# Kernel optimization log

Hardware: AMD Instinct MI355X
Metric: run time of the kernel (lower is better)

## Reference

```python
import jax, jax.numpy as jnp
import numpy as np

F_DIM = 256; L = 4; B = 1; H = 160; W = 160; FH = 1024; N = B * H * W

def _ln(x, w, b):
    mu = jnp.mean(x, -1, keepdims=True)
    var = jnp.mean(jnp.square(x - mu), -1, keepdims=True)
    return (x - mu) * jax.lax.rsqrt(var + 1e-5) * w + b

def _conv(x, w, b, groups=1, pad=0):
    y = jax.lax.conv_general_dilated(x, w, (1, 1), [(pad, pad), (pad, pad)],
                                     dimension_numbers=('NCHW', 'OIHW', 'NCHW'),
                                     feature_group_count=groups)
    return y + b[None, :, None, None]

def _wsilu(x):
    return jax.nn.sigmoid(4.0 * x) * x

def setup_inputs() -> dict:
    key = jax.random.key(0)
    ks = iter(jax.random.split(key, 40))
    nk = lambda: next(ks)
    s = 1.0 / np.sqrt(F_DIM).astype(np.float32)
    inp = {}
    inp['x'] = jax.random.normal(nk(), (B, 1, H, W), jnp.float32)
    inp['cin_w1'] = jax.random.normal(nk(), (F_DIM, 1, 1, 1), jnp.float32)
    inp['cin_b1'] = jnp.zeros((F_DIM,), jnp.float32)
    inp['cin_w2'] = jax.random.normal(nk(), (F_DIM, 1, 7, 7), jnp.float32) * 0.15
    inp['cin_b2'] = jnp.zeros((F_DIM,), jnp.float32)
    inp['ln0_w'] = jnp.ones((F_DIM,), jnp.float32); inp['ln0_b'] = jnp.zeros((F_DIM,), jnp.float32)
    inp['ln1_w'] = jnp.ones((L, F_DIM), jnp.float32); inp['ln1_b'] = jnp.zeros((L, F_DIM), jnp.float32)
    inp['ln2_w'] = jnp.ones((L, F_DIM), jnp.float32); inp['ln2_b'] = jnp.zeros((L, F_DIM), jnp.float32)
    for n in ['att_tmk', 'att_tmv', 'att_tmr', 'ffn_tmk', 'ffn_tmr']:
        inp[n] = jax.random.uniform(nk(), (L, F_DIM), jnp.float32)
    inp['att_tf'] = jax.random.normal(nk(), (L, F_DIM), jnp.float32) * 0.5
    # time_decay is stored as -exp(raw) by the module's loader
    inp['att_td'] = -jnp.exp(jax.random.normal(nk(), (L, F_DIM), jnp.float32) * 0.5)
    for n in ['att_kw', 'att_vw', 'att_rw', 'att_ow', 'ffn_rw']:
        inp[n] = jax.random.normal(nk(), (L, F_DIM, F_DIM), jnp.float32) * s
    inp['ffn_kw'] = jax.random.normal(nk(), (L, FH, F_DIM), jnp.float32) * s
    inp['ffn_vw'] = jax.random.normal(nk(), (L, F_DIM, FH), jnp.float32) * (1.0 / np.sqrt(FH).astype(np.float32))
    inp['spa_dw_w'] = jax.random.normal(nk(), (L, F_DIM, 1, 7, 7), jnp.float32) * 0.15
    inp['spa_dw_b'] = jnp.zeros((L, F_DIM), jnp.float32)
    inp['spa_pw_w'] = jax.random.normal(nk(), (L, F_DIM, F_DIM, 1, 1), jnp.float32) * s
    inp['spa_pw_b'] = jnp.zeros((L, F_DIM), jnp.float32)
    st = jnp.zeros((5 * L, N, F_DIM), jnp.float32)
    st = st.at[4::5].add(-1e30)  # pp slots start at -1e30 as in torch init
    inp['state0'] = st
    return inp

def reference(x, cin_w1, cin_b1, cin_w2, cin_b2, ln0_w, ln0_b, ln1_w, ln1_b,
              ln2_w, ln2_b, att_tmk, att_tmv, att_tmr, att_tf, att_td,
              att_kw, att_vw, att_rw, att_ow, ffn_tmk, ffn_tmr, ffn_kw,
              ffn_vw, ffn_rw, spa_dw_w, spa_dw_b, spa_pw_w, spa_pw_b, state0):
    # conv stem: 1x1 -> depthwise 7x7 -> WSiLU
    d = _conv(x, cin_w1, cin_b1)
    d = _wsilu(_conv(d, cin_w2, cin_b2, groups=F_DIM, pad=3))
    d = d.transpose(0, 2, 3, 1).reshape(N, F_DIM)  # 'b f h w -> (b h w) f'
    for i in range(L):
        if i == 0:
            d = _ln(d, ln0_w, ln0_b)
        # --- SA: single-step RWKV WKV ---
        xs = _ln(d, ln1_w[i], ln1_b[i])
        sp = state0[5 * i + 1]
        aa = state0[5 * i + 2]; bb = state0[5 * i + 3]; pp = state0[5 * i + 4]
        xk = xs * att_tmk[i] + sp * (1 - att_tmk[i])
        xv = xs * att_tmv[i] + sp * (1 - att_tmv[i])
        xr = xs * att_tmr[i] + sp * (1 - att_tmr[i])
        r = jax.nn.sigmoid(xr @ att_rw[i].T)
        k = xk @ att_kw[i].T
        v = xv @ att_vw[i].T
        ww = att_tf[i] + k
        p = jnp.maximum(pp, ww)
        e1 = jnp.exp(pp - p); e2 = jnp.exp(ww - p)
        wkv = (e1 * aa + e2 * v) / (e1 * bb + e2)
        d = d + (r * wkv) @ att_ow[i].T
        # --- FF: squared-relu channel mix ---
        xs = _ln(d, ln2_w[i], ln2_b[i])
        sp = state0[5 * i + 0]
        xk = xs * ffn_tmk[i] + sp * (1 - ffn_tmk[i])
        xr = xs * ffn_tmr[i] + sp * (1 - ffn_tmr[i])
        rr = jax.nn.sigmoid(xr @ ffn_rw[i].T)
        kk = jnp.square(jax.nn.relu(xk @ ffn_kw[i].T))
        d = d + rr * (kk @ ffn_vw[i].T)
        # --- spatial residual block ---
        img = d.reshape(B, H, W, F_DIM).transpose(0, 3, 1, 2)
        img = img + _conv(_conv(img, spa_dw_w[i], spa_dw_b[i], groups=F_DIM, pad=3),
                          spa_pw_w[i], spa_pw_b[i])
        d = img.transpose(0, 2, 3, 1).reshape(N, F_DIM)
    return d.reshape(B, H, W, F_DIM).transpose(0, 3, 1, 2)
```

## Files before the change

### kernel.cpp

```cpp
#include <hip/hip_runtime.h>
#include <hip/hip_bf16.h>
#include <cstdint>
#include <cstddef>

#define F_DIMC 256
#define FHC    1024
#define IMGH   160
#define IMGW   160
#define NTOK   25600
#define NLAY   4

using bf16 = __hip_bfloat16;
using f16  = _Float16;
typedef __attribute__((ext_vector_type(8))) short bf16x8;
typedef __attribute__((ext_vector_type(4))) float f32x4;

#define MFMA16(a, b, c) __builtin_amdgcn_mfma_f32_16x16x32_bf16((a), (b), (c), 0, 0, 0)

union H4 { f16 h[4]; uint2 u; };
union Pack4 { bf16 h[4]; uint2 u; };

struct Cvt6 { const float* s[6]; bf16* d[6]; };
__global__ void cvt6_k(Cvt6 a, int n) {
    int z = blockIdx.y;
    int i = blockIdx.x * 256 + threadIdx.x;
    if (i < n) a.d[z][i] = __float2bfloat16(a.s[z][i]);
}
struct Cvt2 { const float* s[2]; bf16* d[2]; };
__global__ void cvt2_k(Cvt2 a, int n) {
    int z = blockIdx.y;
    int i = blockIdx.x * 256 + threadIdx.x;
    if (i < n) a.d[z][i] = __float2bfloat16(a.s[z][i]);
}

__global__ void dw_transpose_k(const float* __restrict__ src, float* __restrict__ dst, int n) {
    int i = blockIdx.x * 256 + threadIdx.x;
    if (i < n) {
        int f = i & (F_DIMC - 1);
        int lt = i >> 8;
        int t = lt % 49;
        int l = lt / 49;
        dst[i] = src[((size_t)l * F_DIMC + f) * 49 + t];
    }
}

__global__ __launch_bounds__(256)
void stem2_k(const float* __restrict__ x, const float* __restrict__ w1,
             const float* __restrict__ b1, const float* __restrict__ w2,
             const float* __restrict__ b2, f16* __restrict__ d)
{
    __shared__ float wts[49][64];
    __shared__ float w1s[64], b1s[64], b2s[64];
    __shared__ float2 xp[7][22];
    const int tid = threadIdx.x;
    const int f0 = blockIdx.y * 64;
    const int y = blockIdx.x / 10;
    const int x0 = (blockIdx.x % 10) * 16;

    for (int idx = tid; idx < 49 * 64; idx += 256) {
        int t = idx >> 6, fl = idx & 63;
        wts[t][fl] = w2[(f0 + fl) * 49 + t];
    }
    if (tid < 64) {
        w1s[tid] = w1[f0 + tid];
        b1s[tid] = b1[f0 + tid];
        b2s[tid] = b2[f0 + tid];
    }
    for (int p = tid; p < 7 * 22; p += 256) {
        int py = p / 22, px = p % 22;
        int gy = y + py - 3, gx = x0 + px - 3;
        bool ok = (unsigned)gy < IMGH && (unsigned)gx < IMGW;
        xp[py][px] = ok ? make_float2(x[gy * IMGW + gx], 1.f) : make_float2(0.f, 0.f);
    }
    __syncthreads();

    const int fl = tid & 63;
    const int xbase = (tid >> 6) * 4;
    float acc[4] = {0.f, 0.f, 0.f, 0.f}, accw[4] = {0.f, 0.f, 0.f, 0.f};
    #pragma unroll
    for (int ky = 0; ky < 7; ++ky) {
        float2 row[10];
        #pragma unroll
        for (int q = 0; q < 10; ++q) row[q] = xp[ky][xbase + q];
        #pragma unroll
        for (int kx = 0; kx < 7; ++kx) {
            float w = wts[ky * 7 + kx][fl];
            #pragma unroll
            for (int j = 0; j < 4; ++j) {
                acc[j]  = fmaf(row[j + kx].x, w, acc[j]);
                accw[j] = fmaf(row[j + kx].y, w, accw[j]);
            }
        }
    }
    const float w1f = w1s[fl], b1f = b1s[fl], b2f = b2s[fl];
    #pragma unroll
    for (int j = 0; j < 4; ++j) {
        float u = fmaf(w1f, acc[j], fmaf(b1f, accw[j], b2f));
        int pix = y * IMGW + x0 + xbase + j;
        d[(size_t)pix * F_DIMC + f0 + fl] = (f16)(u / (1.f + __expf(-4.f * u)));
    }
}

__device__ __forceinline__ void wave_ln(float* x, const float* __restrict__ w,
                                        const float* __restrict__ b, int lane)
{
    float s = x[0] + x[1] + x[2] + x[3];
    #pragma unroll
    for (int m = 1; m < 64; m <<= 1) s += __shfl_xor(s, m, 64);
    float mu = s * 0.00390625f;
    float t0 = x[0] - mu, t1 = x[1] - mu, t2 = x[2] - mu, t3 = x[3] - mu;
    float v = t0 * t0 + t1 * t1 + t2 * t2 + t3 * t3;
    #pragma unroll
    for (int m = 1; m < 64; m <<= 1) v += __shfl_xor(v, m, 64);
    float inv = rsqrtf(v * 0.00390625f + 1e-5f);
    f32x4 wv = *(const f32x4*)(w + lane * 4);
    f32x4 bv = *(const f32x4*)(b + lane * 4);
    x[0] = t0 * inv * wv[0] + bv[0];
    x[1] = t1 * inv * wv[1] + bv[1];
    x[2] = t2 * inv * wv[2] + bv[2];
    x[3] = t3 * inv * wv[3] + bv[3];
}

template<bool LN0>
__global__ __launch_bounds__(256)
void lnmix_sa_k(f16* __restrict__ d, const float* __restrict__ sp,
                const float* __restrict__ ln0w, const float* __restrict__ ln0b,
                const float* __restrict__ lnw, const float* __restrict__ lnb,
                const float* __restrict__ tmk, const float* __restrict__ tmv,
                const float* __restrict__ tmr,
                bf16* __restrict__ xk, bf16* __restrict__ xv, bf16* __restrict__ xr)
{
    const int lane = threadIdx.x & 63;
    const int n = blockIdx.x * 4 + (threadIdx.x >> 6);
    const int base = n * F_DIMC + lane * 4;
    H4 hv; hv.u = *(const uint2*)(d + base);
    float xo[4] = {(float)hv.h[0], (float)hv.h[1], (float)hv.h[2], (float)hv.h[3]};
    if (LN0) {
        wave_ln(xo, ln0w, ln0b, lane);
        H4 o;
        #pragma unroll
        for (int j = 0; j < 4; ++j) o.h[j] = (f16)xo[j];
        *(uint2*)(d + base) = o.u;
    }
    float xs[4] = {xo[0], xo[1], xo[2], xo[3]};
    wave_ln(xs, lnw, lnb, lane);
    f32x4 spv = *(const f32x4*)(sp + base);
    f32x4 k4 = *(const f32x4*)(tmk + lane * 4);
    f32x4 v4 = *(const f32x4*)(tmv + lane * 4);
    f32x4 r4 = *(const f32x4*)(tmr + lane * 4);
    Pack4 pk, pv, pr;
    #pragma unroll
    for (int j = 0; j < 4; ++j) {
        pk.h[j] = __float2bfloat16(xs[j] * k4[j] + spv[j] * (1.f - k4[j]));
        pv.h[j] = __float2bfloat16(xs[j] * v4[j] + spv[j] * (1.f - v4[j]));
        pr.h[j] = __float2bfloat16(xs[j] * r4[j] + spv[j] * (1.f - r4[j]));
    }
    *(uint2*)(xk + base) = pk.u;
    *(uint2*)(xv + base) = pv.u;
    *(uint2*)(xr + base) = pr.u;
}

__global__ __launch_bounds__(256)
void lnmix_ff_k(const f16* __restrict__ d, const float* __restrict__ sp,
                const float* __restrict__ lnw, const float* __restrict__ lnb,
                const float* __restrict__ tmk, const float* __restrict__ tmr,
                bf16* __restrict__ xk, bf16* __restrict__ xr)
{
    const int lane = threadIdx.x & 63;
    const int n = blockIdx.x * 4 + (threadIdx.x >> 6);
    const int base = n * F_DIMC + lane * 4;
    H4 hv; hv.u = *(const uint2*)(d + base);
    float xs[4] = {(float)hv.h[0], (float)hv.h[1], (float)hv.h[2], (float)hv.h[3]};
    wave_ln(xs, lnw, lnb, lane);
    f32x4 spv = *(const f32x4*)(sp + base);
    f32x4 k4 = *(const f32x4*)(tmk + lane * 4);
    f32x4 r4 = *(const f32x4*)(tmr + lane * 4);
    Pack4 pk, pr;
    #pragma unroll
    for (int j = 0; j < 4; ++j) {
        pk.h[j] = __float2bfloat16(xs[j] * k4[j] + spv[j] * (1.f - k4[j]));
        pr.h[j] = __float2bfloat16(xs[j] * r4[j] + spv[j] * (1.f - r4[j]));
    }
    *(uint2*)(xk + base) = pk.u;
    *(uint2*)(xr + base) = pr.u;
}

__global__ __launch_bounds__(256)
void wkv_k(const f16* __restrict__ r_, const f16* __restrict__ k_,
           const f16* __restrict__ v_, const float* __restrict__ aa,
           const float* __restrict__ bb, const float* __restrict__ pp,
           const float* __restrict__ tf, bf16* __restrict__ out)
{
    int i = blockIdx.x * 256 + threadIdx.x;
    int f0 = (i << 2) & (F_DIMC - 1);
    H4 r4; r4.u = *(const uint2*)(r_ + (size_t)i * 4);
    H4 k4; k4.u = *(const uint2*)(k_ + (size_t)i * 4);
    H4 v4; v4.u = *(const uint2*)(v_ + (size_t)i * 4);
    f32x4 a4 = *(const f32x4*)(aa + (size_t)i * 4);
    f32x4 b4 = *(const f32x4*)(bb + (size_t)i * 4);
    f32x4 p4 = *(const f32x4*)(pp + (size_t)i * 4);
    f32x4 t4 = *(const f32x4*)(tf + f0);
    Pack4 po;
    #pragma unroll
    for (int j = 0; j < 4; ++j) {
        float ww = t4[j] + (float)k4.h[j];
        float p = fmaxf(p4[j], ww);
        float e1 = __expf(p4[j] - p);
        float e2 = __expf(ww - p);
        float wkv = (e1 * a4[j] + e2 * (float)v4.h[j]) / (e1 * b4[j] + e2);
        po.h[j] = __float2bfloat16((float)r4.h[j] * wkv);
    }
    *(uint2*)(out + (size_t)i * 4) = po.u;
}

__device__ __forceinline__ void stage_swz16(const bf16* __restrict__ g, int lda,
                                            bf16* lds, int tid)
{
    #pragma unroll
    for (int s = 0; s < 8; ++s) {
        int chunk = s * 256 + tid;
        int row = chunk >> 4, c16 = chunk & 15;
        int gc = c16 ^ (row & 15);
        __builtin_amdgcn_global_load_lds(
            (const __attribute__((address_space(1))) void*)(g + (size_t)row * lda + gc * 8),
            (__attribute__((address_space(3))) void*)(lds + chunk * 8), 16, 0, 0);
    }
}

template<int RB>
__device__ __forceinline__ bf16x8 frag_ld(const bf16* lds, int row, int cb)
{
    return *(const bf16x8*)((const char*)lds + row * RB + (cb ^ ((row & 15) << 4)));
}

struct G3 { const bf16* A[3]; const bf16* W[3]; f16* C[3]; };
__global__ __launch_bounds__(256, 2)
void gemm3_k(G3 g)
{
    __shared__ __align__(16) bf16 As[128 * 128];
    __shared__ __align__(16) bf16 Bs[128 * 128];
    const int z = blockIdx.z;
    const bf16* __restrict__ A  = g.A[z];
    const bf16* __restrict__ Bw = g.W[z];
    f16* __restrict__ C         = g.C[z];
    const int tid = threadIdx.x, lane = tid & 63, wave = tid >> 6;
    const int wr = wave >> 1, wc = wave & 1;
    const int lr = lane & 15, hi = lane >> 4;
    const int m0 = blockIdx.x * 128, n0 = blockIdx.y * 128;

    f32x4 acc[4][4];
    #pragma unroll
    for (int m = 0; m < 4; ++m)
        #pragma unroll
        for (int n = 0; n < 4; ++n) acc[m][n] = (f32x4){0.f, 0.f, 0.f, 0.f};

    #pragma unroll
    for (int kt = 0; kt < 256; kt += 128) {
        stage_swz16(A + (size_t)m0 * 256 + kt, 256, As, tid);
        stage_swz16(Bw + (size_t)n0 * 256 + kt, 256, Bs, tid);
        __syncthreads();
        #pragma unroll
        for (int ks = 0; ks < 4; ++ks) {
            int cb = ks * 64 + hi * 16;
            bf16x8 a[4], b[4];
            #pragma unroll
            for (int mf = 0; mf < 4; ++mf) a[mf] = frag_ld<256>(As, wr * 64 + mf * 16 + lr, cb);
            #pragma unroll
            for (int nf = 0; nf < 4; ++nf) b[nf] = frag_ld<256>(Bs, wc * 64 + nf * 16 + lr, cb);
            #pragma unroll
            for (int mf = 0; mf < 4; ++mf)
                #pragma unroll
                for (int nf = 0; nf < 4; ++nf)
                    acc[mf][nf] = MFMA16(a[mf], b[nf], acc[mf][nf]);
        }
        __syncthreads();
    }

    const int lr0 = hi * 4;
    #pragma unroll
    for (int mf = 0; mf < 4; ++mf)
        #pragma unroll
        for (int nf = 0; nf < 4; ++nf) {
            int col = n0 + wc * 64 + nf * 16 + lr;
            #pragma unroll
            for (int j = 0; j < 4; ++j) {
                int row = m0 + wr * 64 + mf * 16 + lr0 + j;
                float v = acc[mf][nf][j];
                if (z == 2) v = 1.f / (1.f + __expf(-v));
                C[(size_t)row * F_DIMC + col] = (f16)v;
            }
        }
}

template<int EPI, int K>
__global__ __launch_bounds__(256, 2)
void gemm128_k(const bf16* __restrict__ A, const bf16* __restrict__ Bw,
               int Nout, f16* __restrict__ Cf, bf16* __restrict__ Cb,
               const float* __restrict__ bias)
{
    __shared__ __align__(16) bf16 As[128 * 128];
    __shared__ __align__(16) bf16 Bs[128 * 128];
    const int tid = threadIdx.x, lane = tid & 63, wave = tid >> 6;
    const int wr = wave >> 1, wc = wave & 1;
    const int lr = lane & 15, hi = lane >> 4;
    const int m0 = blockIdx.x * 128, n0 = blockIdx.y * 128;

    f32x4 acc[4][4];
    #pragma unroll
    for (int m = 0; m < 4; ++m)
        #pragma unroll
        for (int n = 0; n < 4; ++n) acc[m][n] = (f32x4){0.f, 0.f, 0.f, 0.f};

    #pragma unroll
    for (int kt = 0; kt < K; kt += 128) {
        stage_swz16(A + (size_t)m0 * K + kt, K, As, tid);
        stage_swz16(Bw + (size_t)n0 * K + kt, K, Bs, tid);
        __syncthreads();
        #pragma unroll
        for (int ks = 0; ks < 4; ++ks) {
            int cb = ks * 64 + hi * 16;
            bf16x8 a[4], b[4];
            #pragma unroll
            for (int mf = 0; mf < 4; ++mf) a[mf] = frag_ld<256>(As, wr * 64 + mf * 16 + lr, cb);
            #pragma unroll
            for (int nf = 0; nf < 4; ++nf) b[nf] = frag_ld<256>(Bs, wc * 64 + nf * 16 + lr, cb);
            #pragma unroll
            for (int mf = 0; mf < 4; ++mf)
                #pragma unroll
                for (int nf = 0; nf < 4; ++nf)
                    acc[mf][nf] = MFMA16(a[mf], b[nf], acc[mf][nf]);
        }
        __syncthreads();
    }

    const int lr0 = hi * 4;
    #pragma unroll
    for (int mf = 0; mf < 4; ++mf)
        #pragma unroll
        for (int nf = 0; nf < 4; ++nf) {
            int col = n0 + wc * 64 + nf * 16 + lr;
            #pragma unroll
            for (int j = 0; j < 4; ++j) {
                int row = m0 + wr * 64 + mf * 16 + lr0 + j;
                size_t cidx = (size_t)row * Nout + col;
                float v = acc[mf][nf][j];
                if constexpr (EPI == 2) { float t = fmaxf(v, 0.f); Cb[cidx] = __float2bfloat16(t * t); }
                else if constexpr (EPI == 3) Cf[cidx] = (f16)((float)Cf[cidx] + v);
                else if constexpr (EPI == 5) Cf[cidx] = (f16)((float)Cf[cidx] + v + bias[col]);
            }
        }
}

__global__ __launch_bounds__(256, 2)
void fvwrr_k(const bf16* __restrict__ kkb, const bf16* __restrict__ fvw,
             const bf16* __restrict__ xr, const bf16* __restrict__ rw,
             f16* __restrict__ d)
{
    __shared__ __align__(16) bf16 As[128 * 128];
    __shared__ __align__(16) bf16 Bs[128 * 128];
    const int tid = threadIdx.x, lane = tid & 63, wave = tid >> 6;
    const int wr = wave >> 1, wc = wave & 1;
    const int lr = lane & 15, hi = lane >> 4;
    const int m0 = blockIdx.x * 128, n0 = blockIdx.y * 128;

    f32x4 arr[4][4], am[4][4];
    #pragma unroll
    for (int m = 0; m < 4; ++m)
        #pragma unroll
        for (int n = 0; n < 4; ++n) {
            arr[m][n] = (f32x4){0.f, 0.f, 0.f, 0.f};
            am[m][n]  = (f32x4){0.f, 0.f, 0.f, 0.f};
        }

    #pragma unroll
    for (int kt = 0; kt < 256; kt += 128) {
        stage_swz16(xr + (size_t)m0 * 256 + kt, 256, As, tid);
        stage_swz16(rw + (size_t)n0 * 256 + kt, 256, Bs, tid);
        __syncthreads();
        #pragma unroll
        for (int ks = 0; ks < 4; ++ks) {
            int cb = ks * 64 + hi * 16;
            bf16x8 a[4], b[4];
            #pragma unroll
            for (int mf = 0; mf < 4; ++mf) a[mf] = frag_ld<256>(As, wr * 64 + mf * 16 + lr, cb);
            #pragma unroll
            for (int nf = 0; nf < 4; ++nf) b[nf] = frag_ld<256>(Bs, wc * 64 + nf * 16 + lr, cb);
            #pragma unroll
            for (int mf = 0; mf < 4; ++mf)
                #pragma unroll
                for (int nf = 0; nf < 4; ++nf)
                    arr[mf][nf] = MFMA16(a[mf], b[nf], arr[mf][nf]);
        }
        __syncthreads();
    }
    #pragma unroll
    for (int kt = 0; kt < 1024; kt += 128) {
        stage_swz16(kkb + (size_t)m0 * 1024 + kt, 1024, As, tid);
        stage_swz16(fvw + (size_t)n0 * 1024 + kt, 1024, Bs, tid);
        __syncthreads();
        #pragma unroll
        for (int ks = 0; ks < 4; ++ks) {
            int cb = ks * 64 + hi * 16;
            bf16x8 a[4], b[4];
            #pragma unroll
            for (int mf = 0; mf < 4; ++mf) a[mf] = frag_ld<256>(As, wr * 64 + mf * 16 + lr, cb);
            #pragma unroll
            for (int nf = 0; nf < 4; ++nf) b[nf] = frag_ld<256>(Bs, wc * 64 + nf * 16 + lr, cb);
            #pragma unroll
            for (int mf = 0; mf < 4; ++mf)
                #pragma unroll
                for (int nf = 0; nf < 4; ++nf)
                    am[mf][nf] = MFMA16(a[mf], b[nf], am[mf][nf]);
        }
        __syncthreads();
    }

    const int lr0 = hi * 4;
    #pragma unroll
    for (int mf = 0; mf < 4; ++mf)
        #pragma unroll
        for (int nf = 0; nf < 4; ++nf) {
            int col = n0 + wc * 64 + nf * 16 + lr;
            #pragma unroll
            for (int j = 0; j < 4; ++j) {
                int row = m0 + wr * 64 + mf * 16 + lr0 + j;
                size_t cidx = (size_t)row * F_DIMC + col;
                float rr = 1.f / (1.f + __expf(-arr[mf][nf][j]));
                d[cidx] = (f16)((float)d[cidx] + rr * am[mf][nf][j]);
            }
        }
}

__global__ __launch_bounds__(256)
void dwconv2_k(const f16* __restrict__ d, const float* __restrict__ wT,
               const float* __restrict__ bias, bf16* __restrict__ out)
{
    __shared__ float patch[196][64];
    __shared__ float wt[49][64];
    const int lane = threadIdx.x;
    const int ty = threadIdx.y;
    const int f0 = blockIdx.z * 64;
    const int w0 = blockIdx.x * 8, h0 = blockIdx.y * 8;

    for (int t = ty; t < 49; t += 4) wt[t][lane] = wT[t * F_DIMC + f0 + lane];
    for (int p = ty; p < 196; p += 4) {
        int py = p / 14, px = p % 14;
        int gy = h0 + py - 3, gx = w0 + px - 3;
        float v = 0.f;
        if ((unsigned)gy < IMGH && (unsigned)gx < IMGW)
            v = (float)d[(size_t)(gy * IMGW + gx) * F_DIMC + f0 + lane];
        patch[p][lane] = v;
    }
    __syncthreads();

    const float b = bias[f0 + lane];
    #pragma unroll
    for (int rr = 0; rr < 2; ++rr) {
        int ry = ty * 2 + rr;
        float acc8[8];
        #pragma unroll
        for (int px = 0; px < 8; ++px) acc8[px] = b;
        #pragma unroll
        for (int ky = 0; ky < 7; ++ky) {
            float rowv[14];
            #pragma unroll
            for (int c = 0; c < 14; ++c) rowv[c] = patch[(ry + ky) * 14 + c][lane];
            #pragma unroll
            for (int kx = 0; kx < 7; ++kx) {
                float w = wt[ky * 7 + kx][lane];
                #pragma unroll
                for (int px = 0; px < 8; ++px)
                    acc8[px] = fmaf(rowv[px + kx], w, acc8[px]);
            }
        }
        #pragma unroll
        for (int px = 0; px < 8; ++px)
            out[(size_t)((h0 + ry) * IMGW + (w0 + px)) * F_DIMC + f0 + lane] = __float2bfloat16(acc8[px]);
    }
}

__global__ __launch_bounds__(256)
void transpose_out_k(const f16* __restrict__ d, float* __restrict__ out)
{
    __shared__ float tile[32][33];
    const int n0 = blockIdx.x * 32, f0 = blockIdx.y * 32;
    const int tx = threadIdx.x, ty = threadIdx.y;
    for (int r = ty; r < 32; r += 8) tile[r][tx] = (float)d[(size_t)(n0 + r) * F_DIMC + f0 + tx];
    __syncthreads();
    for (int r = ty; r < 32; r += 8) out[(size_t)(f0 + r) * NTOK + n0 + tx] = tile[tx][r];
}

extern "C" void kernel_launch(void* const* d_in, const int* in_sizes, int n_in,
                              void* d_out, int out_size, void* d_ws, size_t ws_size,
                              hipStream_t stream)
{
    if (n_in < 30) return;
    const float* x        = (const float*)d_in[0];
    const float* cin_w1   = (const float*)d_in[1];
    const float* cin_b1   = (const float*)d_in[2];
    const float* cin_w2   = (const float*)d_in[3];
    const float* cin_b2   = (const float*)d_in[4];
    const float* ln0_w    = (const float*)d_in[5];
    const float* ln0_b    = (const float*)d_in[6];
    const float* ln1_w    = (const float*)d_in[7];
    const float* ln1_b    = (const float*)d_in[8];
    const float* ln2_w    = (const float*)d_in[9];
    const float* ln2_b    = (const float*)d_in[10];
    const float* att_tmk  = (const float*)d_in[11];
    const float* att_tmv  = (const float*)d_in[12];
    const float* att_tmr  = (const float*)d_in[13];
    const float* ffn_tmk  = (const float*)d_in[14];
    const float* ffn_tmr  = (const float*)d_in[15];
    const float* att_tf   = (const float*)d_in[16];
    const float* att_kw   = (const float*)d_in[18];
    const float* att_vw   = (const float*)d_in[19];
    const float* att_rw   = (const float*)d_in[20];
    const float* att_ow   = (const float*)d_in[21];
    const float* ffn_rw   = (const float*)d_in[22];
    const float* ffn_kw   = (const float*)d_in[23];
    const float* ffn_vw   = (const float*)d_in[24];
    const float* spa_dw_w = (const float*)d_in[25];
    const float* spa_dw_b = (const float*)d_in[26];
    const float* spa_pw_w = (const float*)d_in[27];
    const float* spa_pw_b = (const float*)d_in[28];
    const float* state0   = (const float*)d_in[29];
    float* out = (float*)d_out;

    const size_t NF = (size_t)NTOK * F_DIMC;
    char* wsp = (char*)d_ws;
    size_t off = 0;
    auto alloc = [&](size_t bytes) -> void* {
        void* p = wsp + off;
        off += (bytes + 255) & ~(size_t)255;
        return p;
    };
    f16*   d_buf = (f16*)alloc(NF * 2);
    f16*   Gk    = (f16*)alloc(NF * 2);
    f16*   Gv    = (f16*)alloc(NF * 2);
    f16*   Gr    = (f16*)alloc(NF * 2);
    bf16*  xk    = (bf16*)alloc(NF * 2);
    bf16*  xv    = (bf16*)alloc(NF * 2);
    bf16*  xr    = (bf16*)alloc(NF * 2);
    bf16*  ab    = (bf16*)alloc(NF * 2);
    bf16*  kkb   = (bf16*)alloc((size_t)NTOK * FHC * 2);
    const size_t WSQ = (size_t)NLAY * F_DIMC * F_DIMC;
    bf16* kwb  = (bf16*)alloc(WSQ * 2);
    bf16* vwb  = (bf16*)alloc(WSQ * 2);
    bf16* rwb  = (bf16*)alloc(WSQ * 2);
    bf16* owb  = (bf16*)alloc(WSQ * 2);
    bf16* frwb = (bf16*)alloc(WSQ * 2);
    bf16* fkwb = (bf16*)alloc((size_t)NLAY * FHC * F_DIMC * 2);
    bf16* fvwb = (bf16*)alloc((size_t)NLAY * F_DIMC * FHC * 2);
    bf16* pwb  = (bf16*)alloc(WSQ * 2);
    float* dwT = (float*)alloc((size_t)NLAY * 49 * F_DIMC * 4);
    if (off > ws_size) return;

    {
        Cvt6 c6;
        c6.s[0] = att_kw;  c6.d[0] = kwb;
        c6.s[1] = att_vw;  c6.d[1] = vwb;
        c6.s[2] = att_rw;  c6.d[2] = rwb;
        c6.s[3] = att_ow;  c6.d[3] = owb;
        c6.s[4] = ffn_rw;  c6.d[4] = frwb;
        c6.s[5] = spa_pw_w; c6.d[5] = pwb;
        cvt6_k<<<dim3(((int)WSQ + 255) / 256, 6), dim3(256), 0, stream>>>(c6, (int)WSQ);
        Cvt2 c2;
        c2.s[0] = ffn_kw; c2.d[0] = fkwb;
        c2.s[1] = ffn_vw; c2.d[1] = fvwb;
        int n2 = NLAY * FHC * F_DIMC;
        cvt2_k<<<dim3((n2 + 255) / 256, 2), dim3(256), 0, stream>>>(c2, n2);
        int n = NLAY * 49 * F_DIMC;
        dw_transpose_k<<<dim3((n + 255) / 256), dim3(256), 0, stream>>>(spa_dw_w, dwT, n);
    }

    stem2_k<<<dim3(IMGH * 10, 4), dim3(256), 0, stream>>>(x, cin_w1, cin_b1, cin_w2, cin_b2, d_buf);

    for (int i = 0; i < NLAY; ++i) {
        const float* sp_ff = state0 + (size_t)(5 * i + 0) * NF;
        const float* sp_at = state0 + (size_t)(5 * i + 1) * NF;
        const float* aa    = state0 + (size_t)(5 * i + 2) * NF;
        const float* bb    = state0 + (size_t)(5 * i + 3) * NF;
        const float* pp    = state0 + (size_t)(5 * i + 4) * NF;
        const float* l1w = ln1_w + i * F_DIMC, *l1b = ln1_b + i * F_DIMC;
        const float* l2w = ln2_w + i * F_DIMC, *l2b = ln2_b + i * F_DIMC;
        const float* tmk = att_tmk + i * F_DIMC, *tmv = att_tmv + i * F_DIMC, *tmr = att_tmr + i * F_DIMC;
        const float* ftmk = ffn_tmk + i * F_DIMC, *ftmr = ffn_tmr + i * F_DIMC;
        const float* tf = att_tf + i * F_DIMC;
        const bf16* kw_i  = kwb  + (size_t)i * F_DIMC * F_DIMC;
        const bf16* vw_i  = vwb  + (size_t)i * F_DIMC * F_DIMC;
        const bf16* rw_i  = rwb  + (size_t)i * F_DIMC * F_DIMC;
        const bf16* ow_i  = owb  + (size_t)i * F_DIMC * F_DIMC;
        const bf16* frw_i = frwb + (size_t)i * F_DIMC * F_DIMC;
        const bf16* fkw_i = fkwb + (size_t)i * FHC * F_DIMC;
        const bf16* fvw_i = fvwb + (size_t)i * F_DIMC * FHC;
        const bf16* pw_i  = pwb  + (size_t)i * F_DIMC * F_DIMC;
        const float* dwT_i = dwT + (size_t)i * 49 * F_DIMC;
        const float* dwb_i = spa_dw_b + i * F_DIMC;
        const float* pwbias_i = spa_pw_b + i * F_DIMC;

        if (i == 0)
            lnmix_sa_k<true><<<dim3(NTOK / 4), dim3(256), 0, stream>>>(
                d_buf, sp_at, ln0_w, ln0_b, l1w, l1b, tmk, tmv, tmr, xk, xv, xr);
        else
            lnmix_sa_k<false><<<dim3(NTOK / 4), dim3(256), 0, stream>>>(
                d_buf, sp_at, ln0_w, ln0_b, l1w, l1b, tmk, tmv, tmr, xk, xv, xr);

        G3 g3;
        g3.A[0] = xk; g3.A[1] = xv; g3.A[2] = xr;
        g3.W[0] = kw_i; g3.W[1] = vw_i; g3.W[2] = rw_i;
        g3.C[0] = Gk; g3.C[1] = Gv; g3.C[2] = Gr;
        gemm3_k<<<dim3(NTOK / 128, 2, 3), dim3(256), 0, stream>>>(g3);

        wkv_k<<<dim3((int)(NF / 4 / 256)), dim3(256), 0, stream>>>(Gr, Gk, Gv, aa, bb, pp, tf, ab);

        gemm128_k<3, 256><<<dim3(NTOK / 128, 2), dim3(256), 0, stream>>>(
            ab, ow_i, F_DIMC, d_buf, nullptr, nullptr);

        lnmix_ff_k<<<dim3(NTOK / 4), dim3(256), 0, stream>>>(d_buf, sp_ff, l2w, l2b, ftmk, ftmr, xk, xr);

        gemm128_k<2, 256><<<dim3(NTOK / 128, 8), dim3(256), 0, stream>>>(
            xk, fkw_i, FHC, nullptr, kkb, nullptr);

        fvwrr_k<<<dim3(NTOK / 128, 2), dim3(256), 0, stream>>>(kkb, fvw_i, xr, frw_i, d_buf);

        dwconv2_k<<<dim3(IMGW / 8, IMGH / 8, 4), dim3(64, 4), 0, stream>>>(d_buf, dwT_i, dwb_i, ab);

        gemm128_k<5, 256><<<dim3(NTOK / 128, 2), dim3(256), 0, stream>>>(
            ab, pw_i, F_DIMC, d_buf, nullptr, pwbias_i);
    }

    transpose_out_k<<<dim3(NTOK / 32, F_DIMC / 32), dim3(32, 8), 0, stream>>>(d_buf, out);
}
```

Baseline: 1.931 ms.

## Fold token-mix into GEMM weights and fuse LayerNorm into residual GEMM epilogues

```diff
diff --git a/kernel.cpp b/kernel.cpp
--- a/kernel.cpp
+++ b/kernel.cpp
@@ -20,27 +20,68 @@
 union H4 { f16 h[4]; uint2 u; };
 union Pack4 { bf16 h[4]; uint2 u; };
 
-struct Cvt6 { const float* s[6]; bf16* d[6]; };
-__global__ void cvt6_k(Cvt6 a, int n) {
+__global__ void cvt_sp_k(const float* __restrict__ state0, bf16* __restrict__ spb)
+{
+    const size_t NF = (size_t)NTOK * F_DIMC;
+    int y = blockIdx.y;
+    int slot = (y < 4) ? 5 * y + 1 : 5 * (y - 4);
+    size_t e = ((size_t)blockIdx.x * 256 + threadIdx.x) * 4;
+    f32x4 v = *(const f32x4*)(state0 + (size_t)slot * NF + e);
+    Pack4 p;
+    #pragma unroll
+    for (int j = 0; j < 4; ++j) p.h[j] = __float2bfloat16(v[j]);
+    *(uint2*)(spb + (size_t)y * NF + e) = p.u;
+}
+
+__global__ void prep_mix_k(const float* __restrict__ kw, const float* __restrict__ vw,
+                           const float* __restrict__ rw, const float* __restrict__ tmk,
+                           const float* __restrict__ tmv, const float* __restrict__ tmr,
+                           const float* __restrict__ fkw, const float* __restrict__ ftmk,
+                           const float* __restrict__ frw, const float* __restrict__ ftmr,
+                           bf16* __restrict__ Wcat, bf16* __restrict__ fkw2,
+                           bf16* __restrict__ frw2)
+{
+    int l = blockIdx.y;
+    int idx = blockIdx.x * 256 + threadIdx.x;
+    int c = idx & 511, cc = c & 255;
+    bool hi2 = c >= 256;
+    int r = idx >> 9;
+    if (r < 768) {
+        const float* W; const float* T; int rr = r;
+        if (r < 256)      { W = kw; T = tmk; }
+        else if (r < 512) { W = vw; T = tmv; rr = r - 256; }
+        else              { W = rw; T = tmr; rr = r - 512; }
+        float w = W[(size_t)l * 65536 + rr * 256 + cc];
+        float t = T[l * 256 + cc];
+        Wcat[(size_t)l * 768 * 512 + (size_t)r * 512 + c] = __float2bfloat16(w * (hi2 ? 1.f - t : t));
+    } else if (r < 1792) {
+        int rr = r - 768;
+        float w = fkw[(size_t)l * 1024 * 256 + rr * 256 + cc];
+        float t = ftmk[l * 256 + cc];
+        fkw2[(size_t)l * 1024 * 512 + (size_t)rr * 512 + c] = __float2bfloat16(w * (hi2 ? 1.f - t : t));
+    } else {
+        int rr = r - 1792;
+        float w = frw[(size_t)l * 65536 + rr * 256 + cc];
+        float t = ftmr[l * 256 + cc];
+        frw2[(size_t)l * 256 * 512 + (size_t)rr * 512 + c] = __float2bfloat16(w * (hi2 ? 1.f - t : t));
+    }
+}
+
+__global__ void cvt3_k(const float* __restrict__ ow, const float* __restrict__ pw,
+                       const float* __restrict__ fvw, const float* __restrict__ dww,
+                       bf16* __restrict__ owb, bf16* __restrict__ pwb,
+                       bf16* __restrict__ fvwb, float* __restrict__ dwT)
+{
     int z = blockIdx.y;
     int i = blockIdx.x * 256 + threadIdx.x;
-    if (i < n) a.d[z][i] = __float2bfloat16(a.s[z][i]);
-}
-struct Cvt2 { const float* s[2]; bf16* d[2]; };
-__global__ void cvt2_k(Cvt2 a, int n) {
-    int z = blockIdx.y;
-    int i = blockIdx.x * 256 + threadIdx.x;
-    if (i < n) a.d[z][i] = __float2bfloat16(a.s[z][i]);
-}
-
-__global__ void dw_transpose_k(const float* __restrict__ src, float* __restrict__ dst, int n) {
-    int i = blockIdx.x * 256 + threadIdx.x;
-    if (i < n) {
-        int f = i & (F_DIMC - 1);
-        int lt = i >> 8;
-        int t = lt % 49;
-        int l = lt / 49;
-        dst[i] = src[((size_t)l * F_DIMC + f) * 49 + t];
+    if (z == 0)      { if (i < 262144)  owb[i]  = __float2bfloat16(ow[i]); }
+    else if (z == 1) { if (i < 262144)  pwb[i]  = __float2bfloat16(pw[i]); }
+    else if (z == 2) { if (i < 1048576) fvwb[i] = __float2bfloat16(fvw[i]); }
+    else {
+        if (i < 50176) {
+            int f = i & 255; int lt = i >> 8; int t = lt % 49; int l = lt / 49;
+            dwT[i] = dww[((size_t)l * F_DIMC + f) * 49 + t];
+        }
     }
 }
 
@@ -121,85 +162,44 @@
     x[3] = t3 * inv * wv[3] + bv[3];
 }
 
-template<bool LN0>
 __global__ __launch_bounds__(256)
-void lnmix_sa_k(f16* __restrict__ d, const float* __restrict__ sp,
-                const float* __restrict__ ln0w, const float* __restrict__ ln0b,
-                const float* __restrict__ lnw, const float* __restrict__ lnb,
-                const float* __restrict__ tmk, const float* __restrict__ tmv,
-                const float* __restrict__ tmr,
-                bf16* __restrict__ xk, bf16* __restrict__ xv, bf16* __restrict__ xr)
+void ln_first_k(f16* __restrict__ d, const float* __restrict__ ln0w,
+                const float* __restrict__ ln0b, const float* __restrict__ l1w,
+                const float* __restrict__ l1b, bf16* __restrict__ xs)
 {
     const int lane = threadIdx.x & 63;
     const int n = blockIdx.x * 4 + (threadIdx.x >> 6);
     const int base = n * F_DIMC + lane * 4;
     H4 hv; hv.u = *(const uint2*)(d + base);
     float xo[4] = {(float)hv.h[0], (float)hv.h[1], (float)hv.h[2], (float)hv.h[3]};
-    if (LN0) {
-        wave_ln(xo, ln0w, ln0b, lane);
-        H4 o;
-        #pragma unroll
-        for (int j = 0; j < 4; ++j) o.h[j] = (f16)xo[j];
-        *(uint2*)(d + base) = o.u;
-    }
-    float xs[4] = {xo[0], xo[1], xo[2], xo[3]};
-    wave_ln(xs, lnw, lnb, lane);
-    f32x4 spv = *(const f32x4*)(sp + base);
-    f32x4 k4 = *(const f32x4*)(tmk + lane * 4);
-    f32x4 v4 = *(const f32x4*)(tmv + lane * 4);
-    f32x4 r4 = *(const f32x4*)(tmr + lane * 4);
-    Pack4 pk, pv, pr;
-    #pragma unroll
-    for (int j = 0; j < 4; ++j) {
-        pk.h[j] = __float2bfloat16(xs[j] * k4[j] + spv[j] * (1.f - k4[j]));
-        pv.h[j] = __float2bfloat16(xs[j] * v4[j] + spv[j] * (1.f - v4[j]));
-        pr.h[j] = __float2bfloat16(xs[j] * r4[j] + spv[j] * (1.f - r4[j]));
-    }
-    *(uint2*)(xk + base) = pk.u;
-    *(uint2*)(xv + base) = pv.u;
-    *(uint2*)(xr + base) = pr.u;
+    wave_ln(xo, ln0w, ln0b, lane);
+    H4 o;
+    #pragma unroll
+    for (int j = 0; j < 4; ++j) o.h[j] = (f16)xo[j];
+    *(uint2*)(d + base) = o.u;
+    wave_ln(xo, l1w, l1b, lane);
+    Pack4 p;
+    #pragma unroll
+    for (int j = 0; j < 4; ++j) p.h[j] = __float2bfloat16(xo[j]);
+    *(uint2*)(xs + base) = p.u;
 }
 
 __global__ __launch_bounds__(256)
-void lnmix_ff_k(const f16* __restrict__ d, const float* __restrict__ sp,
-                const float* __restrict__ lnw, const float* __restrict__ lnb,
-                const float* __restrict__ tmk, const float* __restrict__ tmr,
-                bf16* __restrict__ xk, bf16* __restrict__ xr)
-{
-    const int lane = threadIdx.x & 63;
-    const int n = blockIdx.x * 4 + (threadIdx.x >> 6);
-    const int base = n * F_DIMC + lane * 4;
-    H4 hv; hv.u = *(const uint2*)(d + base);
-    float xs[4] = {(float)hv.h[0], (float)hv.h[1], (float)hv.h[2], (float)hv.h[3]};
-    wave_ln(xs, lnw, lnb, lane);
-    f32x4 spv = *(const f32x4*)(sp + base);
-    f32x4 k4 = *(const f32x4*)(tmk + lane * 4);
-    f32x4 r4 = *(const f32x4*)(tmr + lane * 4);
-    Pack4 pk, pr;
-    #pragma unroll
-    for (int j = 0; j < 4; ++j) {
-        pk.h[j] = __float2bfloat16(xs[j] * k4[j] + spv[j] * (1.f - k4[j]));
-        pr.h[j] = __float2bfloat16(xs[j] * r4[j] + spv[j] * (1.f - r4[j]));
-    }
-    *(uint2*)(xk + base) = pk.u;
-    *(uint2*)(xr + base) = pr.u;
-}
-
-__global__ __launch_bounds__(256)
-void wkv_k(const f16* __restrict__ r_, const f16* __restrict__ k_,
-           const f16* __restrict__ v_, const float* __restrict__ aa,
+void wkv_k(const f16* __restrict__ G, const float* __restrict__ aa,
            const float* __restrict__ bb, const float* __restrict__ pp,
-           const float* __restrict__ tf, bf16* __restrict__ out)
-{
-    int i = blockIdx.x * 256 + threadIdx.x;
-    int f0 = (i << 2) & (F_DIMC - 1);
-    H4 r4; r4.u = *(const uint2*)(r_ + (size_t)i * 4);
-    H4 k4; k4.u = *(const uint2*)(k_ + (size_t)i * 4);
-    H4 v4; v4.u = *(const uint2*)(v_ + (size_t)i * 4);
-    f32x4 a4 = *(const f32x4*)(aa + (size_t)i * 4);
-    f32x4 b4 = *(const f32x4*)(bb + (size_t)i * 4);
-    f32x4 p4 = *(const f32x4*)(pp + (size_t)i * 4);
-    f32x4 t4 = *(const f32x4*)(tf + f0);
+           const float* __restrict__ tf, bf16* __restrict__ ab)
+{
+    size_t i = (size_t)blockIdx.x * 256 + threadIdx.x;
+    size_t e = i * 4;
+    int row = (int)(e >> 8), c = (int)(e & 255);
+    const f16* g = G + (size_t)row * 768 + c;
+    H4 k4; k4.u = *(const uint2*)(g);
+    H4 v4; v4.u = *(const uint2*)(g + 256);
+    H4 r4; r4.u = *(const uint2*)(g + 512);
+    f32x4 a4 = *(const f32x4*)(aa + e);
+    f32x4 b4 = *(const f32x4*)(bb + e);
+    f32x4 p4 = *(const f32x4*)(pp + e);
+    f32x4 t4 = *(const f32x4*)(tf + c);
     Pack4 po;
     #pragma unroll
     for (int j = 0; j < 4; ++j) {
@@ -208,9 +208,10 @@
         float e1 = __expf(p4[j] - p);
         float e2 = __expf(ww - p);
         float wkv = (e1 * a4[j] + e2 * (float)v4.h[j]) / (e1 * b4[j] + e2);
-        po.h[j] = __float2bfloat16((float)r4.h[j] * wkv);
-    }
-    *(uint2*)(out + (size_t)i * 4) = po.u;
+        float rs = 1.f / (1.f + __expf(-(float)r4.h[j]));
+        po.h[j] = __float2bfloat16(rs * wkv);
+    }
+    *(uint2*)(ab + e) = po.u;
 }
 
 __device__ __forceinline__ void stage_swz16(const bf16* __restrict__ g, int lda,
@@ -226,77 +227,33 @@
             (__attribute__((address_space(3))) void*)(lds + chunk * 8), 16, 0, 0);
     }
 }
+__device__ __forceinline__ void stage_swz8(const bf16* __restrict__ g, int lda,
+                                           bf16* lds, int tid, int nloads)
+{
+    #pragma unroll
+    for (int s = 0; s < 8; ++s) {
+        if (s >= nloads) break;
+        int chunk = s * 256 + tid;
+        int row = chunk >> 3, c = chunk & 7;
+        int gc = c ^ (row & 7);
+        __builtin_amdgcn_global_load_lds(
+            (const __attribute__((address_space(1))) void*)(g + (size_t)row * lda + gc * 8),
+            (__attribute__((address_space(3))) void*)(lds + chunk * 8), 16, 0, 0);
+    }
+}
 
 template<int RB>
 __device__ __forceinline__ bf16x8 frag_ld(const bf16* lds, int row, int cb)
 {
-    return *(const bf16x8*)((const char*)lds + row * RB + (cb ^ ((row & 15) << 4)));
-}
-
-struct G3 { const bf16* A[3]; const bf16* W[3]; f16* C[3]; };
+    constexpr int M = (RB >= 256) ? 15 : (RB / 16 - 1);
+    return *(const bf16x8*)((const char*)lds + row * RB + (cb ^ ((row & M) << 4)));
+}
+
+template<int EPI, int K, bool SPLITA>
 __global__ __launch_bounds__(256, 2)
-void gemm3_k(G3 g)
-{
-    __shared__ __align__(16) bf16 As[128 * 128];
-    __shared__ __align__(16) bf16 Bs[128 * 128];
-    const int z = blockIdx.z;
-    const bf16* __restrict__ A  = g.A[z];
-    const bf16* __restrict__ Bw = g.W[z];
-    f16* __restrict__ C         = g.C[z];
-    const int tid = threadIdx.x, lane = tid & 63, wave = tid >> 6;
-    const int wr = wave >> 1, wc = wave & 1;
-    const int lr = lane & 15, hi = lane >> 4;
-    const int m0 = blockIdx.x * 128, n0 = blockIdx.y * 128;
-
-    f32x4 acc[4][4];
-    #pragma unroll
-    for (int m = 0; m < 4; ++m)
-        #pragma unroll
-        for (int n = 0; n < 4; ++n) acc[m][n] = (f32x4){0.f, 0.f, 0.f, 0.f};
-
-    #pragma unroll
-    for (int kt = 0; kt < 256; kt += 128) {
-        stage_swz16(A + (size_t)m0 * 256 + kt, 256, As, tid);
-        stage_swz16(Bw + (size_t)n0 * 256 + kt, 256, Bs, tid);
-        __syncthreads();
-        #pragma unroll
-        for (int ks = 0; ks < 4; ++ks) {
-            int cb = ks * 64 + hi * 16;
-            bf16x8 a[4], b[4];
-            #pragma unroll
-            for (int mf = 0; mf < 4; ++mf) a[mf] = frag_ld<256>(As, wr * 64 + mf * 16 + lr, cb);
-            #pragma unroll
-            for (int nf = 0; nf < 4; ++nf) b[nf] = frag_ld<256>(Bs, wc * 64 + nf * 16 + lr, cb);
-            #pragma unroll
-            for (int mf = 0; mf < 4; ++mf)
-                #pragma unroll
-                for (int nf = 0; nf < 4; ++nf)
-                    acc[mf][nf] = MFMA16(a[mf], b[nf], acc[mf][nf]);
-        }
-        __syncthreads();
-    }
-
-    const int lr0 = hi * 4;
-    #pragma unroll
-    for (int mf = 0; mf < 4; ++mf)
-        #pragma unroll
-        for (int nf = 0; nf < 4; ++nf) {
-            int col = n0 + wc * 64 + nf * 16 + lr;
-            #pragma unroll
-            for (int j = 0; j < 4; ++j) {
-                int row = m0 + wr * 64 + mf * 16 + lr0 + j;
-                float v = acc[mf][nf][j];
-                if (z == 2) v = 1.f / (1.f + __expf(-v));
-                C[(size_t)row * F_DIMC + col] = (f16)v;
-            }
-        }
-}
-
-template<int EPI, int K>
-__global__ __launch_bounds__(256, 2)
-void gemm128_k(const bf16* __restrict__ A, const bf16* __restrict__ Bw,
-               int Nout, f16* __restrict__ Cf, bf16* __restrict__ Cb,
-               const float* __restrict__ bias)
+void gemm128_k(const bf16* __restrict__ A1, const bf16* __restrict__ A2,
+               const bf16* __restrict__ Bw, int ldb, int Nout,
+               f16* __restrict__ Cf, bf16* __restrict__ Cb)
 {
     __shared__ __align__(16) bf16 As[128 * 128];
     __shared__ __align__(16) bf16 Bs[128 * 128];
@@ -313,8 +270,13 @@
 
     #pragma unroll
     for (int kt = 0; kt < K; kt += 128) {
-        stage_swz16(A + (size_t)m0 * K + kt, K, As, tid);
-        stage_swz16(Bw + (size_t)n0 * K + kt, K, Bs, tid);
+        const bf16* Ap;
+        if constexpr (SPLITA)
+            Ap = (kt < 256) ? (A1 + (size_t)m0 * 256 + kt) : (A2 + (size_t)m0 * 256 + (kt - 256));
+        else
+            Ap = A1 + (size_t)m0 * K + kt;
+        stage_swz16(Ap, SPLITA ? 256 : K, As, tid);
+        stage_swz16(Bw + (size_t)n0 * ldb + kt, ldb, Bs, tid);
         __syncthreads();
         #pragma unroll
         for (int ks = 0; ks < 4; ++ks) {
@@ -344,17 +306,113 @@
                 int row = m0 + wr * 64 + mf * 16 + lr0 + j;
                 size_t cidx = (size_t)row * Nout + col;
                 float v = acc[mf][nf][j];
-                if constexpr (EPI == 2) { float t = fmaxf(v, 0.f); Cb[cidx] = __float2bfloat16(t * t); }
-                else if constexpr (EPI == 3) Cf[cidx] = (f16)((float)Cf[cidx] + v);
-                else if constexpr (EPI == 5) Cf[cidx] = (f16)((float)Cf[cidx] + v + bias[col]);
+                if constexpr (EPI == 0) Cf[cidx] = (f16)v;
+                else if constexpr (EPI == 2) { float t = fmaxf(v, 0.f); Cb[cidx] = __float2bfloat16(t * t); }
             }
         }
+}
+
+template<bool BIAS, bool DOLN>
+__global__ __launch_bounds__(256, 2)
+void gemmln_k(const bf16* __restrict__ A, const bf16* __restrict__ W,
+              f16* __restrict__ d, bf16* __restrict__ xs,
+              const float* __restrict__ lnw, const float* __restrict__ lnb,
+              const float* __restrict__ bias)
+{
+    __shared__ __align__(16) bf16 As[64 * 64];
+    __shared__ __align__(16) bf16 Bs[256 * 64];
+    __shared__ float2 lnp[64][4];
+    const int tid = threadIdx.x, lane = tid & 63, wave = tid >> 6;
+    const int lr = lane & 15, hi = lane >> 4;
+    const int m0 = blockIdx.x * 64;
+
+    f32x4 acc[4][4];
+    #pragma unroll
+    for (int m = 0; m < 4; ++m)
+        #pragma unroll
+        for (int n = 0; n < 4; ++n) acc[m][n] = (f32x4){0.f, 0.f, 0.f, 0.f};
+
+    #pragma unroll
+    for (int kt = 0; kt < 256; kt += 64) {
+        stage_swz8(A + (size_t)m0 * 256 + kt, 256, As, tid, 2);
+        stage_swz8(W + kt, 256, Bs, tid, 8);
+        __syncthreads();
+        #pragma unroll
+        for (int ks = 0; ks < 2; ++ks) {
+            int cb = ks * 64 + hi * 16;
+            bf16x8 a[4], b[4];
+            #pragma unroll
+            for (int mf = 0; mf < 4; ++mf) a[mf] = frag_ld<128>(As, mf * 16 + lr, cb);
+            #pragma unroll
+            for (int nf = 0; nf < 4; ++nf) b[nf] = frag_ld<128>(Bs, wave * 64 + nf * 16 + lr, cb);
+            #pragma unroll
+            for (int mf = 0; mf < 4; ++mf)
+                #pragma unroll
+                for (int nf = 0; nf < 4; ++nf)
+                    acc[mf][nf] = MFMA16(a[mf], b[nf], acc[mf][nf]);
+        }
+        __syncthreads();
+    }
+
+    const int lr0 = hi * 4;
+    #pragma unroll
+    for (int mf = 0; mf < 4; ++mf) {
+        #pragma unroll
+        for (int j = 0; j < 4; ++j) {
+            int row = m0 + mf * 16 + lr0 + j;
+            float s = 0.f, q = 0.f;
+            #pragma unroll
+            for (int nf = 0; nf < 4; ++nf) {
+                int col = wave * 64 + nf * 16 + lr;
+                size_t ci = (size_t)row * F_DIMC + col;
+                float v = acc[mf][nf][j] + (float)d[ci];
+                if constexpr (BIAS) v += bias[col];
+                acc[mf][nf][j] = v;
+                d[ci] = (f16)v;
+                s += v; q += v * v;
+            }
+            if constexpr (DOLN) {
+                #pragma unroll
+                for (int m = 1; m < 16; m <<= 1) {
+                    s += __shfl_xor(s, m, 64);
+                    q += __shfl_xor(q, m, 64);
+                }
+                if (lr == 0) lnp[mf * 16 + lr0 + j][wave] = make_float2(s, q);
+            }
+        }
+    }
+    if constexpr (DOLN) {
+        __syncthreads();
+        #pragma unroll
+        for (int mf = 0; mf < 4; ++mf) {
+            #pragma unroll
+            for (int j = 0; j < 4; ++j) {
+                int ri = mf * 16 + lr0 + j;
+                float S = 0.f, Q = 0.f;
+                #pragma unroll
+                for (int w2 = 0; w2 < 4; ++w2) {
+                    float2 p = lnp[ri][w2];
+                    S += p.x; Q += p.y;
+                }
+                float mu = S * 0.00390625f;
+                float var = Q * 0.00390625f - mu * mu;
+                float inv = rsqrtf(var + 1e-5f);
+                int row = m0 + ri;
+                #pragma unroll
+                for (int nf = 0; nf < 4; ++nf) {
+                    int col = wave * 64 + nf * 16 + lr;
+                    float v = (acc[mf][nf][j] - mu) * inv * lnw[col] + lnb[col];
+                    xs[(size_t)row * F_DIMC + col] = __float2bfloat16(v);
+                }
+            }
+        }
+    }
 }
 
 __global__ __launch_bounds__(256, 2)
 void fvwrr_k(const bf16* __restrict__ kkb, const bf16* __restrict__ fvw,
-             const bf16* __restrict__ xr, const bf16* __restrict__ rw,
-             f16* __restrict__ d)
+             const bf16* __restrict__ xs, const bf16* __restrict__ sp,
+             const bf16* __restrict__ frw2, f16* __restrict__ d)
 {
     __shared__ __align__(16) bf16 As[128 * 128];
     __shared__ __align__(16) bf16 Bs[128 * 128];
@@ -373,9 +431,10 @@
         }
 
     #pragma unroll
-    for (int kt = 0; kt < 256; kt += 128) {
-        stage_swz16(xr + (size_t)m0 * 256 + kt, 256, As, tid);
-        stage_swz16(rw + (size_t)n0 * 256 + kt, 256, Bs, tid);
+    for (int kt = 0; kt < 512; kt += 128) {
+        const bf16* Ap = (kt < 256) ? (xs + (size_t)m0 * 256 + kt) : (sp + (size_t)m0 * 256 + (kt - 256));
+        stage_swz16(Ap, 256, As, tid);
+        stage_swz16(frw2 + (size_t)n0 * 512 + kt, 512, Bs, tid);
         __syncthreads();
         #pragma unroll
         for (int ks = 0; ks < 4; ++ks) {
@@ -535,98 +594,63 @@
         return p;
     };
     f16*   d_buf = (f16*)alloc(NF * 2);
-    f16*   Gk    = (f16*)alloc(NF * 2);
-    f16*   Gv    = (f16*)alloc(NF * 2);
-    f16*   Gr    = (f16*)alloc(NF * 2);
-    bf16*  xk    = (bf16*)alloc(NF * 2);
-    bf16*  xv    = (bf16*)alloc(NF * 2);
-    bf16*  xr    = (bf16*)alloc(NF * 2);
+    bf16*  xs    = (bf16*)alloc(NF * 2);
+    f16*   G     = (f16*)alloc((size_t)NTOK * 768 * 2);
     bf16*  ab    = (bf16*)alloc(NF * 2);
     bf16*  kkb   = (bf16*)alloc((size_t)NTOK * FHC * 2);
-    const size_t WSQ = (size_t)NLAY * F_DIMC * F_DIMC;
-    bf16* kwb  = (bf16*)alloc(WSQ * 2);
-    bf16* vwb  = (bf16*)alloc(WSQ * 2);
-    bf16* rwb  = (bf16*)alloc(WSQ * 2);
-    bf16* owb  = (bf16*)alloc(WSQ * 2);
-    bf16* frwb = (bf16*)alloc(WSQ * 2);
-    bf16* fkwb = (bf16*)alloc((size_t)NLAY * FHC * F_DIMC * 2);
-    bf16* fvwb = (bf16*)alloc((size_t)NLAY * F_DIMC * FHC * 2);
-    bf16* pwb  = (bf16*)alloc(WSQ * 2);
-    float* dwT = (float*)alloc((size_t)NLAY * 49 * F_DIMC * 4);
+    bf16*  spb   = (bf16*)alloc(8 * NF * 2);
+    bf16*  Wcat  = (bf16*)alloc((size_t)NLAY * 768 * 512 * 2);
+    bf16*  fkw2  = (bf16*)alloc((size_t)NLAY * 1024 * 512 * 2);
+    bf16*  frw2  = (bf16*)alloc((size_t)NLAY * 256 * 512 * 2);
+    bf16*  owb   = (bf16*)alloc((size_t)NLAY * 65536 * 2);
+    bf16*  pwb   = (bf16*)alloc((size_t)NLAY * 65536 * 2);
+    bf16*  fvwb  = (bf16*)alloc((size_t)NLAY * 262144 * 2);
+    float* dwT   = (float*)alloc((size_t)NLAY * 49 * F_DIMC * 4);
     if (off > ws_size) return;
 
-    {
-        Cvt6 c6;
-        c6.s[0] = att_kw;  c6.d[0] = kwb;
-        c6.s[1] = att_vw;  c6.d[1] = vwb;
-        c6.s[2] = att_rw;  c6.d[2] = rwb;
-        c6.s[3] = att_ow;  c6.d[3] = owb;
-        c6.s[4] = ffn_rw;  c6.d[4] = frwb;
-        c6.s[5] = spa_pw_w; c6.d[5] = pwb;
-        cvt6_k<<<dim3(((int)WSQ + 255) / 256, 6), dim3(256), 0, stream>>>(c6, (int)WSQ);
-        Cvt2 c2;
-        c2.s[0] = ffn_kw; c2.d[0] = fkwb;
-        c2.s[1] = ffn_vw; c2.d[1] = fvwb;
-        int n2 = NLAY * FHC * F_DIMC;
-        cvt2_k<<<dim3((n2 + 255) / 256, 2), dim3(256), 0, stream>>>(c2, n2);
-        int n = NLAY * 49 * F_DIMC;
-        dw_transpose_k<<<dim3((n + 255) / 256), dim3(256), 0, stream>>>(spa_dw_w, dwT, n);
-    }
+    cvt_sp_k<<<dim3((int)(NF / 1024), 8), dim3(256), 0, stream>>>(state0, spb);
+    prep_mix_k<<<dim3(4096, 4), dim3(256), 0, stream>>>(
+        att_kw, att_vw, att_rw, att_tmk, att_tmv, att_tmr,
+        ffn_kw, ffn_tmk, ffn_rw, ffn_tmr, Wcat, fkw2, frw2);
+    cvt3_k<<<dim3(4096, 4), dim3(256), 0, stream>>>(
+        att_ow, spa_pw_w, ffn_vw, spa_dw_w, owb, pwb, fvwb, dwT);
 
     stem2_k<<<dim3(IMGH * 10, 4), dim3(256), 0, stream>>>(x, cin_w1, cin_b1, cin_w2, cin_b2, d_buf);
+    ln_first_k<<<dim3(NTOK / 4), dim3(256), 0, stream>>>(d_buf, ln0_w, ln0_b, ln1_w, ln1_b, xs);
 
     for (int i = 0; i < NLAY; ++i) {
-        const float* sp_ff = state0 + (size_t)(5 * i + 0) * NF;
-        const float* sp_at = state0 + (size_t)(5 * i + 1) * NF;
-        const float* aa    = state0 + (size_t)(5 * i + 2) * NF;
-        const float* bb    = state0 + (size_t)(5 * i + 3) * NF;
-        const float* pp    = state0 + (size_t)(5 * i + 4) * NF;
-        const float* l1w = ln1_w + i * F_DIMC, *l1b = ln1_b + i * F_DIMC;
-        const float* l2w = ln2_w + i * F_DIMC, *l2b = ln2_b + i * F_DIMC;
-        const float* tmk = att_tmk + i * F_DIMC, *tmv = att_tmv + i * F_DIMC, *tmr = att_tmr + i * F_DIMC;
-        const float* ftmk = ffn_tmk + i * F_DIMC, *ftmr = ffn_tmr + i * F_DIMC;
+        const float* aa = state0 + (size_t)(5 * i + 2) * NF;
+        const float* bb = state0 + (size_t)(5 * i + 3) * NF;
+        const float* pp = state0 + (size_t)(5 * i + 4) * NF;
         const float* tf = att_tf + i * F_DIMC;
-        const bf16* kw_i  = kwb  + (size_t)i * F_DIMC * F_DIMC;
-        const bf16* vw_i  = vwb  + (size_t)i * F_DIMC * F_DIMC;
-        const bf16* rw_i  = rwb  + (size_t)i * F_DIMC * F_DIMC;
-        const bf16* ow_i  = owb  + (size_t)i * F_DIMC * F_DIMC;
-        const bf16* frw_i = frwb + (size_t)i * F_DIMC * F_DIMC;
-        const bf16* fkw_i = fkwb + (size_t)i * FHC * F_DIMC;
-        const bf16* fvw_i = fvwb + (size_t)i * F_DIMC * FHC;
-        const bf16* pw_i  = pwb  + (size_t)i * F_DIMC * F_DIMC;
+        const bf16* sp_at = spb + (size_t)i * NF;
+        const bf16* sp_ff = spb + (size_t)(4 + i) * NF;
+        const bf16* Wcat_i = Wcat + (size_t)i * 768 * 512;
+        const bf16* fkw2_i = fkw2 + (size_t)i * 1024 * 512;
+        const bf16* frw2_i = frw2 + (size_t)i * 256 * 512;
+        const bf16* ow_i   = owb  + (size_t)i * 65536;
+        const bf16* pw_i   = pwb  + (size_t)i * 65536;
+        const bf16* fvw_i  = fvwb + (size_t)i * 262144;
         const float* dwT_i = dwT + (size_t)i * 49 * F_DIMC;
         const float* dwb_i = spa_dw_b + i * F_DIMC;
         const float* pwbias_i = spa_pw_b + i * F_DIMC;
 
-        if (i == 0)
-            lnmix_sa_k<true><<<dim3(NTOK / 4), dim3(256), 0, stream>>>(
-                d_buf, sp_at, ln0_w, ln0_b, l1w, l1b, tmk, tmv, tmr, xk, xv, xr);
+        gemm128_k<0, 512, true><<<dim3(NTOK / 128, 6), dim3(256), 0, stream>>>(
+            xs, sp_at, Wcat_i, 512, 768, G, nullptr);
+        wkv_k<<<dim3((int)(NF / 1024)), dim3(256), 0, stream>>>(G, aa, bb, pp, tf, ab);
+        gemmln_k<false, true><<<dim3(NTOK / 64), dim3(256), 0, stream>>>(
+            ab, ow_i, d_buf, xs, ln2_w + i * F_DIMC, ln2_b + i * F_DIMC, nullptr);
+        gemm128_k<2, 512, true><<<dim3(NTOK / 128, 8), dim3(256), 0, stream>>>(
+            xs, sp_ff, fkw2_i, 512, 1024, nullptr, kkb);
+        fvwrr_k<<<dim3(NTOK / 128, 2), dim3(256), 0, stream>>>(
+            kkb, fvw_i, xs, sp_ff, frw2_i, d_buf);
+        dwconv2_k<<<dim3(IMGW / 8, IMGH / 8, 4), dim3(64, 4), 0, stream>>>(d_buf, dwT_i, dwb_i, ab);
+        if (i < NLAY - 1)
+            gemmln_k<true, true><<<dim3(NTOK / 64), dim3(256), 0, stream>>>(
+                ab, pw_i, d_buf, xs, ln1_w + (i + 1) * F_DIMC, ln1_b + (i + 1) * F_DIMC, pwbias_i);
         else
-            lnmix_sa_k<false><<<dim3(NTOK / 4), dim3(256), 0, stream>>>(
-                d_buf, sp_at, ln0_w, ln0_b, l1w, l1b, tmk, tmv, tmr, xk, xv, xr);
-
-        G3 g3;
-        g3.A[0] = xk; g3.A[1] = xv; g3.A[2] = xr;
-        g3.W[0] = kw_i; g3.W[1] = vw_i; g3.W[2] = rw_i;
-        g3.C[0] = Gk; g3.C[1] = Gv; g3.C[2] = Gr;
-        gemm3_k<<<dim3(NTOK / 128, 2, 3), dim3(256), 0, stream>>>(g3);
-
-        wkv_k<<<dim3((int)(NF / 4 / 256)), dim3(256), 0, stream>>>(Gr, Gk, Gv, aa, bb, pp, tf, ab);
-
-        gemm128_k<3, 256><<<dim3(NTOK / 128, 2), dim3(256), 0, stream>>>(
-            ab, ow_i, F_DIMC, d_buf, nullptr, nullptr);
-
-        lnmix_ff_k<<<dim3(NTOK / 4), dim3(256), 0, stream>>>(d_buf, sp_ff, l2w, l2b, ftmk, ftmr, xk, xr);
-
-        gemm128_k<2, 256><<<dim3(NTOK / 128, 8), dim3(256), 0, stream>>>(
-            xk, fkw_i, FHC, nullptr, kkb, nullptr);
-
-        fvwrr_k<<<dim3(NTOK / 128, 2), dim3(256), 0, stream>>>(kkb, fvw_i, xr, frw_i, d_buf);
-
-        dwconv2_k<<<dim3(IMGW / 8, IMGH / 8, 4), dim3(64, 4), 0, stream>>>(d_buf, dwT_i, dwb_i, ab);
-
-        gemm128_k<5, 256><<<dim3(NTOK / 128, 2), dim3(256), 0, stream>>>(
-            ab, pw_i, F_DIMC, d_buf, nullptr, pwbias_i);
+            gemmln_k<true, false><<<dim3(NTOK / 64), dim3(256), 0, stream>>>(
+                ab, pw_i, d_buf, xs, nullptr, nullptr, pwbias_i);
     }
 
     transpose_out_k<<<dim3(NTOK / 32, F_DIMC / 32), dim3(32, 8), 0, stream>>>(d_buf, out);
```

Measured after the change: 1.999 ms. 3.5% more time.
